# Performance work log

Measured on AMD Instinct MI355X. Metric: run time of the kernel, lower is better.

## Reference

```python
import jax, jax.numpy as jnp
import numpy as np
import math

S, B, D = 2048, 2, 1024
H = 16
DH = D // H
WIN = 256
DIL = 1


def setup_inputs() -> dict:
    key = jax.random.key(0)
    ks = jax.random.split(key, 10)
    std = 1.0 / math.sqrt(D)
    return {
        "x": jax.random.normal(ks[0], (S, B, D), jnp.float32),
        "beta": jax.random.normal(ks[1], (H,), jnp.float32) * 0.02,
        "Wq": jax.random.normal(ks[2], (D, D), jnp.float32) * std,
        "bq": jnp.zeros((D,), jnp.float32),
        "Wk": jax.random.normal(ks[3], (D, D), jnp.float32) * std,
        "bk": jnp.zeros((D,), jnp.float32),
        "Wv": jax.random.normal(ks[4], (D, D), jnp.float32) * std,
        "bv": jnp.zeros((D,), jnp.float32),
        "Wo": jax.random.normal(ks[5], (D, D), jnp.float32) * std,
        "bo": jnp.zeros((D,), jnp.float32),
    }


def _split_heads(t):
    # (S, B, D) -> (B*H, S, DH), matching rearrange 's b (h d) -> (b h) s d'
    return t.reshape(S, B, H, DH).transpose(1, 2, 0, 3).reshape(B * H, S, DH)


def reference(x, beta, Wq, bq, Wk, bk, Wv, bv, Wo, bo):
    q = _split_heads(x @ Wq + bq)
    k = _split_heads(x @ Wk + bk)
    v = _split_heads(x @ Wv + bv)

    # per-head learnable temperature: q / (sqrt(d_head) * exp(beta))
    beta_exp = jnp.tile(jnp.exp(beta), B)  # (B*H,), head index = z % H
    q = q / (jnp.sqrt(jnp.asarray(DH, x.dtype)) * beta_exp)[:, None, None]

    # causal dilated windowed mask
    idx = jnp.arange(S)
    diff = idx[:, None] - idx[None, :]
    allowed = (diff >= 0) & (diff <= DIL * (WIN - 1)) & (diff % DIL == 0)
    mask = jnp.where(allowed, jnp.asarray(0.0, x.dtype), jnp.asarray(-jnp.inf, x.dtype))

    scores = jnp.einsum('zqd,zkd->zqk', q, k) + mask[None]
    # attention sink: extra zero-logit column absorbing probability mass
    scores = jnp.concatenate([scores, jnp.zeros((B * H, S, 1), scores.dtype)], axis=-1)
    attn = jax.nn.softmax(scores, axis=-1)[..., :-1]

    out = jnp.einsum('zqk,zkd->zqd', attn, v)
    # (B*H, S, DH) -> (S, B, D)
    out = out.reshape(B, H, S, DH).transpose(2, 0, 1, 3).reshape(S, B, D)
    return out @ Wo + bo
```

## Files before the change

kernel.cpp:

```cpp
#include <hip/hip_runtime.h>
#include <math.h>

#define S_LEN  2048
#define BATCH  2
#define DM     1024
#define NHEAD  16
#define DHEAD  64
#define WIN    256
#define MROWS  4096

#define KP   72
#define PPAD 68

#define BM 256
#define BN 192
#define BK 64

#define OM 128
#define ON 128

typedef __attribute__((ext_vector_type(8))) short bf16x8;
typedef __attribute__((ext_vector_type(4))) float f32x4;

__device__ __forceinline__ unsigned short f2b(float f) {
    unsigned int u = __float_as_uint(f);
    return (unsigned short)((u + 0x7fffu + ((u >> 16) & 1u)) >> 16);
}
__device__ __forceinline__ void gld16(const void* g, void* l) {
    __builtin_amdgcn_global_load_lds(
        (const __attribute__((address_space(1))) void*)g,
        (__attribute__((address_space(3))) void*)l, 16, 0, 0);
}
__device__ __forceinline__ bf16x8 pack8(float4 a, float4 b) {
    bf16x8 r;
    r[0] = (short)f2b(a.x); r[1] = (short)f2b(a.y);
    r[2] = (short)f2b(a.z); r[3] = (short)f2b(a.w);
    r[4] = (short)f2b(b.x); r[5] = (short)f2b(b.y);
    r[6] = (short)f2b(b.z); r[7] = (short)f2b(b.w);
    return r;
}

__global__ __launch_bounds__(256)
void cvtx(const float* __restrict__ x, unsigned short* __restrict__ xb)
{
    const int i = (blockIdx.x * 256 + threadIdx.x) * 4;
    float4 f = *(const float4*)(x + i);
    ushort4 o; o.x = f2b(f.x); o.y = f2b(f.y); o.z = f2b(f.z); o.w = f2b(f.w);
    *(ushort4*)(xb + i) = o;
}

__global__ __launch_bounds__(256)
void twcvt4(const float* __restrict__ W0, const float* __restrict__ W1,
            const float* __restrict__ W2, const float* __restrict__ W3,
            unsigned short* __restrict__ T0, unsigned short* __restrict__ T1,
            unsigned short* __restrict__ T2, unsigned short* __restrict__ T3)
{
    const int zz = blockIdx.z;
    const float* W = (zz == 0) ? W0 : (zz == 1) ? W1 : (zz == 2) ? W2 : W3;
    unsigned short* WT = (zz == 0) ? T0 : (zz == 1) ? T1 : (zz == 2) ? T2 : T3;

    __shared__ float t32[32][33];
    const int bx = blockIdx.x * 32;
    const int by = blockIdx.y * 32;
    const int c  = threadIdx.x & 31;
    const int r0 = threadIdx.x >> 5;
#pragma unroll
    for (int p = 0; p < 4; ++p)
        t32[r0 + 8 * p][c] = W[(size_t)(by + r0 + 8 * p) * DM + bx + c];
    __syncthreads();
#pragma unroll
    for (int p = 0; p < 4; ++p)
        WT[(size_t)(bx + r0 + 8 * p) * DM + by + c] = f2b(t32[c][r0 + 8 * p]);
}

__global__ __launch_bounds__(512, 2)
void gemm_qkv(const unsigned short* __restrict__ A,
              const unsigned short* __restrict__ BT,
              const float* __restrict__ b0,
              const float* __restrict__ b1,
              const float* __restrict__ b2,
              const float* __restrict__ beta,
              unsigned short* __restrict__ Cb)
{
    __shared__ unsigned short Ab[2][BM * BK];
    __shared__ unsigned short Bb[2][BN * BK];

    const int t   = threadIdx.x;
    const int ln  = t & 63;
    const int wv  = t >> 6;
    const int wr  = wv & 3;
    const int wc  = wv >> 2;
    const int m16 = ln & 15;
    const int g   = ln >> 4;
    const int sw  = m16 & 7;

    const int rowBase = blockIdx.y * BM;
    const int colBase = blockIdx.x * BN;

    const int sr  = t >> 3;
    const int scx = (t & 7) ^ (sr & 7);
    const size_t gOff = (size_t)sr * DM + scx * 8;
    const int    ldOff = t * 8;

    f32x4 acc[4][6];
#pragma unroll
    for (int u = 0; u < 4; ++u)
#pragma unroll
        for (int v = 0; v < 6; ++v)
            acc[u][v] = (f32x4){0.f, 0.f, 0.f, 0.f};

    {
        const unsigned short* a0 = A  + (size_t)rowBase * DM + gOff;
        const unsigned short* bt = BT + (size_t)colBase * DM + gOff;
#pragma unroll
        for (int cb = 0; cb < 3; ++cb)
            gld16(bt + (size_t)cb * 64 * DM, &Bb[0][cb * 4096 + ldOff]);
#pragma unroll
        for (int ca = 0; ca < 4; ++ca)
            gld16(a0 + (size_t)ca * 64 * DM, &Ab[0][ca * 4096 + ldOff]);
        asm volatile("s_waitcnt vmcnt(0)" ::: "memory");
        __builtin_amdgcn_s_barrier();
        __builtin_amdgcn_sched_barrier(0);
    }

    for (int kt = 0; kt < DM / BK; ++kt) {
        const int cur = kt & 1;
        const unsigned short* Ac = Ab[cur];
        const unsigned short* Bc = Bb[cur];
        unsigned short* An = Ab[cur ^ 1];
        unsigned short* Bn = Bb[cur ^ 1];
        const bool hn = (kt < DM / BK - 1);
        const unsigned short* aS = A  + (size_t)rowBase * DM + (kt + 1) * BK + gOff;
        const unsigned short* bS = BT + (size_t)colBase * DM + (kt + 1) * BK + gOff;

        bf16x8 af0[4], bf0[6];
#pragma unroll
        for (int u = 0; u < 4; ++u)
            af0[u] = *(const bf16x8*)&Ac[(wr * 64 + u * 16 + m16) * BK + ((g ^ sw) * 8)];
#pragma unroll
        for (int v = 0; v < 6; ++v)
            bf0[v] = *(const bf16x8*)&Bc[(wc * 96 + v * 16 + m16) * BK + ((g ^ sw) * 8)];

        if (hn) {
            gld16(bS,                    &Bn[ldOff]);
            gld16(bS + (size_t)64 * DM,  &Bn[4096 + ldOff]);
            gld16(bS + (size_t)128 * DM, &Bn[2 * 4096 + ldOff]);
            gld16(aS,                    &An[ldOff]);
            gld16(aS + (size_t)64 * DM,  &An[4096 + ldOff]);
            gld16(aS + (size_t)128 * DM, &An[2 * 4096 + ldOff]);
            gld16(aS + (size_t)192 * DM, &An[3 * 4096 + ldOff]);
        }

        __builtin_amdgcn_s_setprio(1);
#pragma unroll
        for (int u = 0; u < 4; ++u)
#pragma unroll
            for (int v = 0; v < 6; ++v)
                acc[u][v] = __builtin_amdgcn_mfma_f32_16x16x32_bf16(
                    af0[u], bf0[v], acc[u][v], 0, 0, 0);
        __builtin_amdgcn_s_setprio(0);

        bf16x8 af1[4], bf1[6];
#pragma unroll
        for (int u = 0; u < 4; ++u)
            af1[u] = *(const bf16x8*)&Ac[(wr * 64 + u * 16 + m16) * BK + (((4 | g) ^ sw) * 8)];
#pragma unroll
        for (int v = 0; v < 6; ++v)
            bf1[v] = *(const bf16x8*)&Bc[(wc * 96 + v * 16 + m16) * BK + (((4 | g) ^ sw) * 8)];

        __builtin_amdgcn_s_setprio(1);
#pragma unroll
        for (int u = 0; u < 4; ++u)
#pragma unroll
            for (int v = 0; v < 6; ++v)
                acc[u][v] = __builtin_amdgcn_mfma_f32_16x16x32_bf16(
                    af1[u], bf1[v], acc[u][v], 0, 0, 0);
        __builtin_amdgcn_s_setprio(0);

        if (hn)
            asm volatile("s_waitcnt vmcnt(0)" ::: "memory");
        __builtin_amdgcn_s_barrier();
        __builtin_amdgcn_sched_barrier(0);
    }

    const int q4 = g * 4;
#pragma unroll
    for (int v = 0; v < 6; ++v) {
        const int col = colBase + wc * 96 + v * 16 + m16;
        const int sec = col >> 10;
        const int h   = (col >> 6) & (NHEAD - 1);
        const int dh  = col & 63;
        if (sec < 2) {
            const float bi = (sec == 0 ? b0 : b1)[col & (DM - 1)];
            const float sc = (sec == 0) ? 0.125f * __expf(-beta[h]) : 1.0f;
            unsigned short* base = Cb + (size_t)sec * MROWS * DM;
#pragma unroll
            for (int u = 0; u < 4; ++u)
#pragma unroll
                for (int r = 0; r < 4; ++r) {
                    const int row = rowBase + wr * 64 + u * 16 + q4 + r;
                    const int s = row >> 1, bb = row & 1;
                    const int z = bb * NHEAD + h;
                    base[((size_t)z * S_LEN + s) * DHEAD + dh] =
                        f2b((acc[u][v][r] + bi) * sc);
                }
        } else {
            unsigned short* vtb = Cb + (size_t)2 * MROWS * DM;
            const float bi = b2[col & (DM - 1)];
#pragma unroll
            for (int u = 0; u < 4; ++u) {
                const int row0 = rowBase + wr * 64 + u * 16 + q4;
                const int s0   = row0 >> 1;
                ushort2 p0, p1;
                p0.x = f2b(acc[u][v][0] + bi);
                p0.y = f2b(acc[u][v][2] + bi);
                p1.x = f2b(acc[u][v][1] + bi);
                p1.y = f2b(acc[u][v][3] + bi);
                *(ushort2*)(vtb + ((size_t)(h * DHEAD + dh) * S_LEN + s0)) = p0;
                *(ushort2*)(vtb + ((size_t)((NHEAD + h) * DHEAD + dh) * S_LEN + s0)) = p1;
            }
        }
    }
}

__global__ __launch_bounds__(256, 2)
void gemm_out(const unsigned short* __restrict__ A,
              const unsigned short* __restrict__ BT,
              const float* __restrict__ bias,
              float* __restrict__ Cf)
{
    __shared__ unsigned short As[2][OM * BK];
    __shared__ unsigned short Bs[2][ON * BK];

    const int t  = threadIdx.x;
    const int wv = t >> 6, ln = t & 63;
    const int wr = wv >> 1, wc = wv & 1;
    const int m16 = ln & 15, g = ln >> 4;
    const int sw  = m16 & 7;

    const int rowBase = blockIdx.y * OM;
    const int colBase = blockIdx.x * ON;

    const int sr  = t >> 3;
    const int scx = (t & 7) ^ (sr & 7);
    const size_t gOff = (size_t)sr * DM + scx * 8;
    const int    ldOff = t * 8;

    f32x4 acc[4][4];
#pragma unroll
    for (int u = 0; u < 4; ++u)
#pragma unroll
        for (int v = 0; v < 4; ++v)
            acc[u][v] = (f32x4){0.f, 0.f, 0.f, 0.f};

    {
        const unsigned short* a0 = A  + (size_t)rowBase * DM + gOff;
        const unsigned short* bt = BT + (size_t)colBase * DM + gOff;
#pragma unroll
        for (int ca = 0; ca < 2; ++ca)
#pragma unroll
            for (int hf = 0; hf < 2; ++hf)
                gld16(a0 + (size_t)(ca * 64 + hf * 32) * DM,
                      &As[0][ca * 4096 + hf * 2048 + ldOff]);
#pragma unroll
        for (int cb = 0; cb < 2; ++cb)
#pragma unroll
            for (int hf = 0; hf < 2; ++hf)
                gld16(bt + (size_t)(cb * 64 + hf * 32) * DM,
                      &Bs[0][cb * 4096 + hf * 2048 + ldOff]);
        asm volatile("s_waitcnt vmcnt(0)" ::: "memory");
        __builtin_amdgcn_s_barrier();
        __builtin_amdgcn_sched_barrier(0);
    }

    for (int kt = 0; kt < DM / BK; ++kt) {
        const int cur = kt & 1;
        const unsigned short* Ac = As[cur];
        const unsigned short* Bc = Bs[cur];
        unsigned short* An = As[cur ^ 1];
        unsigned short* Bn = Bs[cur ^ 1];
        const bool hn = (kt < DM / BK - 1);
        const unsigned short* aS = A  + (size_t)rowBase * DM + (kt + 1) * BK + gOff;
        const unsigned short* bS = BT + (size_t)colBase * DM + (kt + 1) * BK + gOff;

        bf16x8 af0[4], bf0[4];
#pragma unroll
        for (int u = 0; u < 4; ++u)
            af0[u] = *(const bf16x8*)&Ac[(wr * 64 + u * 16 + m16) * BK + ((g ^ sw) * 8)];
#pragma unroll
        for (int v = 0; v < 4; ++v)
            bf0[v] = *(const bf16x8*)&Bc[(wc * 64 + v * 16 + m16) * BK + ((g ^ sw) * 8)];

        if (hn) {
#pragma unroll
            for (int ca = 0; ca < 2; ++ca)
#pragma unroll
                for (int hf = 0; hf < 2; ++hf)
                    gld16(aS + (size_t)(ca * 64 + hf * 32) * DM,
                          &An[ca * 4096 + hf * 2048 + ldOff]);
#pragma unroll
            for (int cb = 0; cb < 2; ++cb)
#pragma unroll
                for (int hf = 0; hf < 2; ++hf)
                    gld16(bS + (size_t)(cb * 64 + hf * 32) * DM,
                          &Bn[cb * 4096 + hf * 2048 + ldOff]);
        }

        __builtin_amdgcn_s_setprio(1);
#pragma unroll
        for (int u = 0; u < 4; ++u)
#pragma unroll
            for (int v = 0; v < 4; ++v)
                acc[u][v] = __builtin_amdgcn_mfma_f32_16x16x32_bf16(
                    af0[u], bf0[v], acc[u][v], 0, 0, 0);
        __builtin_amdgcn_s_setprio(0);

        bf16x8 af1[4], bf1[4];
#pragma unroll
        for (int u = 0; u < 4; ++u)
            af1[u] = *(const bf16x8*)&Ac[(wr * 64 + u * 16 + m16) * BK + (((4 | g) ^ sw) * 8)];
#pragma unroll
        for (int v = 0; v < 4; ++v)
            bf1[v] = *(const bf16x8*)&Bc[(wc * 64 + v * 16 + m16) * BK + (((4 | g) ^ sw) * 8)];

        __builtin_amdgcn_s_setprio(1);
#pragma unroll
        for (int u = 0; u < 4; ++u)
#pragma unroll
            for (int v = 0; v < 4; ++v)
                acc[u][v] = __builtin_amdgcn_mfma_f32_16x16x32_bf16(
                    af1[u], bf1[v], acc[u][v], 0, 0, 0);
        __builtin_amdgcn_s_setprio(0);

        if (hn)
            asm volatile("s_waitcnt vmcnt(0)" ::: "memory");
        __builtin_amdgcn_s_barrier();
        __builtin_amdgcn_sched_barrier(0);
    }

    const int q4 = g * 4;
#pragma unroll
    for (int v = 0; v < 4; ++v) {
        const int col = colBase + wc * 64 + v * 16 + m16;
        const float bi = bias[col];
#pragma unroll
        for (int u = 0; u < 4; ++u)
#pragma unroll
            for (int r = 0; r < 4; ++r) {
                const int row = rowBase + wr * 64 + u * 16 + q4 + r;
                Cf[(size_t)row * DM + col] = acc[u][v][r] + bi;
            }
    }
}

__global__ __launch_bounds__(256, 4)
void attn_mfma(const unsigned short* __restrict__ q,
               const unsigned short* __restrict__ k,
               const unsigned short* __restrict__ vt,
               unsigned short* __restrict__ ao)
{
    __shared__ unsigned short Ks[64 * KP];
    __shared__ unsigned short Vs[64 * KP];
    __shared__ float Ps[64][PPAD];

    const int t   = threadIdx.x;
    const int wv  = t >> 6, ln = t & 63;
    const int m16 = ln & 15, g = ln >> 4;
    const int z   = blockIdx.y;
    const int q0  = blockIdx.x * 64;
    const size_t zbase = (size_t)z * S_LEN * DHEAD;

    const unsigned short* qrow = q + zbase + (size_t)(q0 + wv * 16 + m16) * DHEAD;
    bf16x8 qf0 = *(const bf16x8*)(qrow + g * 8);
    bf16x8 qf1 = *(const bf16x8*)(qrow + 32 + g * 8);

    f32x4 oacc[4];
#pragma unroll
    for (int v4 = 0; v4 < 4; ++v4) oacc[v4] = (f32x4){0.f, 0.f, 0.f, 0.f};
    float lr[4];
#pragma unroll
    for (int r = 0; r < 4; ++r) lr[r] = 1.f;

    for (int c = 0; c < 5; ++c) {
        const int kb = q0 - 256 + c * 64;
        if (kb < 0) continue;
        __syncthreads();

#pragma unroll
        for (int i = 0; i < 2; ++i) {
            const int id  = t + 256 * i;
            const int row = id >> 3;
            const int co  = (id & 7) * 8;
            *(bf16x8*)&Ks[row * KP + co] =
                *(const bf16x8*)(k + zbase + (size_t)(kb + row) * DHEAD + co);
            *(bf16x8*)&Vs[row * KP + co] =
                *(const bf16x8*)(vt + ((size_t)z * DHEAD + row) * S_LEN + kb + co);
        }
        __syncthreads();

        f32x4 sacc[4];
#pragma unroll
        for (int v4 = 0; v4 < 4; ++v4) {
            sacc[v4] = (f32x4){0.f, 0.f, 0.f, 0.f};
            bf16x8 kf0 = *(const bf16x8*)&Ks[(v4 * 16 + m16) * KP + g * 8];
            sacc[v4] = __builtin_amdgcn_mfma_f32_16x16x32_bf16(qf0, kf0, sacc[v4], 0, 0, 0);
            bf16x8 kf1 = *(const bf16x8*)&Ks[(v4 * 16 + m16) * KP + 32 + g * 8];
            sacc[v4] = __builtin_amdgcn_mfma_f32_16x16x32_bf16(qf1, kf1, sacc[v4], 0, 0, 0);
        }

        const bool mhi = (c == 4), mlo = (c == 0);
#pragma unroll
        for (int r = 0; r < 4; ++r) {
            const int ig = q0 + wv * 16 + g * 4 + r;
            float rsum = 0.f;
#pragma unroll
            for (int v4 = 0; v4 < 4; ++v4) {
                const int jg = kb + v4 * 16 + m16;
                float x = sacc[v4][r];
                const bool valid = (!mhi || jg <= ig) && (!mlo || jg >= ig - (WIN - 1));
                x = valid ? x : -1e30f;
                const float pp = __expf(x);
                Ps[wv * 16 + g * 4 + r][v4 * 16 + m16] = pp;
                rsum += pp;
            }
#pragma unroll
            for (int off = 1; off < 16; off <<= 1)
                rsum += __shfl_xor(rsum, off, 64);
            lr[r] += rsum;
        }
        __syncthreads();

        const float* prow = &Ps[wv * 16 + m16][0];
        bf16x8 pf0 = pack8(*(const float4*)(prow + g * 8),
                           *(const float4*)(prow + g * 8 + 4));
        bf16x8 pf1 = pack8(*(const float4*)(prow + 32 + g * 8),
                           *(const float4*)(prow + 32 + g * 8 + 4));
#pragma unroll
        for (int v4 = 0; v4 < 4; ++v4) {
            bf16x8 vf0 = *(const bf16x8*)&Vs[(v4 * 16 + m16) * KP + g * 8];
            oacc[v4] = __builtin_amdgcn_mfma_f32_16x16x32_bf16(pf0, vf0, oacc[v4], 0, 0, 0);
            bf16x8 vf1 = *(const bf16x8*)&Vs[(v4 * 16 + m16) * KP + 32 + g * 8];
            oacc[v4] = __builtin_amdgcn_mfma_f32_16x16x32_bf16(pf1, vf1, oacc[v4], 0, 0, 0);
        }
    }

    const int bb = z >> 4, h = z & 15;
#pragma unroll
    for (int r = 0; r < 4; ++r) {
        const int ig  = q0 + wv * 16 + g * 4 + r;
        const float inv = 1.f / lr[r];
#pragma unroll
        for (int v4 = 0; v4 < 4; ++v4)
            ao[(size_t)(ig * BATCH + bb) * DM + h * DHEAD + v4 * 16 + m16] =
                f2b(oacc[v4][r] * inv);
    }
}

extern "C" void kernel_launch(void* const* d_in, const int* in_sizes, int n_in,
                              void* d_out, int out_size, void* d_ws, size_t ws_size,
                              hipStream_t stream)
{
    const float* x    = (const float*)d_in[0];
    const float* beta = (const float*)d_in[1];
    const float* Wq   = (const float*)d_in[2];
    const float* bq   = (const float*)d_in[3];
    const float* Wk   = (const float*)d_in[4];
    const float* bk   = (const float*)d_in[5];
    const float* Wv   = (const float*)d_in[6];
    const float* bv   = (const float*)d_in[7];
    const float* Wo   = (const float*)d_in[8];
    const float* bo   = (const float*)d_in[9];
    float* out = (float*)d_out;

    unsigned short* w = (unsigned short*)d_ws;
    const size_t seg = (size_t)MROWS * DM;
    unsigned short* qb  = w;
    unsigned short* kb  = w + seg;
    unsigned short* vtb = w + 2 * seg;
    unsigned short* ab  = w + 3 * seg;
    unsigned short* xb  = w + 4 * seg;
    unsigned short* wtq = w + 5 * seg;
    unsigned short* wtk = wtq + (size_t)DM * DM;
    unsigned short* wtv = wtk + (size_t)DM * DM;
    unsigned short* wto = wtv + (size_t)DM * DM;

    cvtx<<<4096, 256, 0, stream>>>(x, xb);
    twcvt4<<<dim3(32, 32, 4), 256, 0, stream>>>(Wq, Wk, Wv, Wo, wtq, wtk, wtv, wto);

    gemm_qkv<<<dim3(3072 / BN, MROWS / BM), 512, 0, stream>>>(
        xb, wtq, bq, bk, bv, beta, qb);

    attn_mfma<<<dim3(S_LEN / 64, BATCH * NHEAD), 256, 0, stream>>>(qb, kb, vtb, ab);

    gemm_out<<<dim3(DM / ON, MROWS / OM), 256, 0, stream>>>(ab, wto, bo, out);
}
```

Measured before the change: 169.4 us.

## Double-buffer K/V with async LDS loads in attention; halve output GEMM tile width

The attention kernel now stages K and V chunks into double-buffered, XOR-swizzled LDS via direct global-to-LDS loads. The next chunk is prefetched while the current one is computed, and fully masked leading chunks are skipped up front. A block-wide barrier after the probability write is replaced with a wave-local LDS wait, since each wave reads only its own rows. The output projection GEMM tile narrows from 128 to 64 columns to launch more blocks. This trades more LDS per attention block (lower occupancy bound) and less reuse per GEMM block for better overlap and fill.

```diff
diff --git a/kernel.cpp b/kernel.cpp
--- a/kernel.cpp
+++ b/kernel.cpp
@@ -9,7 +9,6 @@
 #define WIN    256
 #define MROWS  4096
 
-#define KP   72
 #define PPAD 68
 
 #define BM 256
@@ -17,7 +16,7 @@
 #define BK 64
 
 #define OM 128
-#define ON 128
+#define ON 64
 
 typedef __attribute__((ext_vector_type(8))) short bf16x8;
 typedef __attribute__((ext_vector_type(4))) float f32x4;
@@ -246,28 +245,22 @@
     const size_t gOff = (size_t)sr * DM + scx * 8;
     const int    ldOff = t * 8;
 
-    f32x4 acc[4][4];
+    f32x4 acc[4][2];
 #pragma unroll
     for (int u = 0; u < 4; ++u)
 #pragma unroll
-        for (int v = 0; v < 4; ++v)
+        for (int v = 0; v < 2; ++v)
             acc[u][v] = (f32x4){0.f, 0.f, 0.f, 0.f};
 
     {
         const unsigned short* a0 = A  + (size_t)rowBase * DM + gOff;
         const unsigned short* bt = BT + (size_t)colBase * DM + gOff;
 #pragma unroll
-        for (int ca = 0; ca < 2; ++ca)
-#pragma unroll
-            for (int hf = 0; hf < 2; ++hf)
-                gld16(a0 + (size_t)(ca * 64 + hf * 32) * DM,
-                      &As[0][ca * 4096 + hf * 2048 + ldOff]);
-#pragma unroll
-        for (int cb = 0; cb < 2; ++cb)
-#pragma unroll
-            for (int hf = 0; hf < 2; ++hf)
-                gld16(bt + (size_t)(cb * 64 + hf * 32) * DM,
-                      &Bs[0][cb * 4096 + hf * 2048 + ldOff]);
+        for (int j = 0; j < 4; ++j)
+            gld16(a0 + (size_t)(j * 32) * DM, &As[0][j * 2048 + ldOff]);
+#pragma unroll
+        for (int j = 0; j < 2; ++j)
+            gld16(bt + (size_t)(j * 32) * DM, &Bs[0][j * 2048 + ldOff]);
         asm volatile("s_waitcnt vmcnt(0)" ::: "memory");
         __builtin_amdgcn_s_barrier();
         __builtin_amdgcn_sched_barrier(0);
@@ -283,51 +276,45 @@
         const unsigned short* aS = A  + (size_t)rowBase * DM + (kt + 1) * BK + gOff;
         const unsigned short* bS = BT + (size_t)colBase * DM + (kt + 1) * BK + gOff;
 
-        bf16x8 af0[4], bf0[4];
+        bf16x8 af0[4], bf0[2];
 #pragma unroll
         for (int u = 0; u < 4; ++u)
             af0[u] = *(const bf16x8*)&Ac[(wr * 64 + u * 16 + m16) * BK + ((g ^ sw) * 8)];
 #pragma unroll
-        for (int v = 0; v < 4; ++v)
-            bf0[v] = *(const bf16x8*)&Bc[(wc * 64 + v * 16 + m16) * BK + ((g ^ sw) * 8)];
+        for (int v = 0; v < 2; ++v)
+            bf0[v] = *(const bf16x8*)&Bc[(wc * 32 + v * 16 + m16) * BK + ((g ^ sw) * 8)];
 
         if (hn) {
 #pragma unroll
-            for (int ca = 0; ca < 2; ++ca)
-#pragma unroll
-                for (int hf = 0; hf < 2; ++hf)
-                    gld16(aS + (size_t)(ca * 64 + hf * 32) * DM,
-                          &An[ca * 4096 + hf * 2048 + ldOff]);
-#pragma unroll
-            for (int cb = 0; cb < 2; ++cb)
-#pragma unroll
-                for (int hf = 0; hf < 2; ++hf)
-                    gld16(bS + (size_t)(cb * 64 + hf * 32) * DM,
-                          &Bn[cb * 4096 + hf * 2048 + ldOff]);
+            for (int j = 0; j < 4; ++j)
+                gld16(aS + (size_t)(j * 32) * DM, &An[j * 2048 + ldOff]);
+#pragma unroll
+            for (int j = 0; j < 2; ++j)
+                gld16(bS + (size_t)(j * 32) * DM, &Bn[j * 2048 + ldOff]);
         }
 
         __builtin_amdgcn_s_setprio(1);
 #pragma unroll
         for (int u = 0; u < 4; ++u)
 #pragma unroll
-            for (int v = 0; v < 4; ++v)
+            for (int v = 0; v < 2; ++v)
                 acc[u][v] = __builtin_amdgcn_mfma_f32_16x16x32_bf16(
                     af0[u], bf0[v], acc[u][v], 0, 0, 0);
         __builtin_amdgcn_s_setprio(0);
 
-        bf16x8 af1[4], bf1[4];
+        bf16x8 af1[4], bf1[2];
 #pragma unroll
         for (int u = 0; u < 4; ++u)
             af1[u] = *(const bf16x8*)&Ac[(wr * 64 + u * 16 + m16) * BK + (((4 | g) ^ sw) * 8)];
 #pragma unroll
-        for (int v = 0; v < 4; ++v)
-            bf1[v] = *(const bf16x8*)&Bc[(wc * 64 + v * 16 + m16) * BK + (((4 | g) ^ sw) * 8)];
+        for (int v = 0; v < 2; ++v)
+            bf1[v] = *(const bf16x8*)&Bc[(wc * 32 + v * 16 + m16) * BK + (((4 | g) ^ sw) * 8)];
 
         __builtin_amdgcn_s_setprio(1);
 #pragma unroll
         for (int u = 0; u < 4; ++u)
 #pragma unroll
-            for (int v = 0; v < 4; ++v)
+            for (int v = 0; v < 2; ++v)
                 acc[u][v] = __builtin_amdgcn_mfma_f32_16x16x32_bf16(
                     af1[u], bf1[v], acc[u][v], 0, 0, 0);
         __builtin_amdgcn_s_setprio(0);
@@ -340,8 +327,8 @@
 
     const int q4 = g * 4;
 #pragma unroll
-    for (int v = 0; v < 4; ++v) {
-        const int col = colBase + wc * 64 + v * 16 + m16;
+    for (int v = 0; v < 2; ++v) {
+        const int col = colBase + wc * 32 + v * 16 + m16;
         const float bi = bias[col];
 #pragma unroll
         for (int u = 0; u < 4; ++u)
@@ -353,23 +340,30 @@
     }
 }
 
-__global__ __launch_bounds__(256, 4)
+__global__ __launch_bounds__(256, 3)
 void attn_mfma(const unsigned short* __restrict__ q,
                const unsigned short* __restrict__ k,
                const unsigned short* __restrict__ vt,
                unsigned short* __restrict__ ao)
 {
-    __shared__ unsigned short Ks[64 * KP];
-    __shared__ unsigned short Vs[64 * KP];
+    __shared__ unsigned short Ks[2][64 * 64];
+    __shared__ unsigned short Vs[2][64 * 64];
     __shared__ float Ps[64][PPAD];
 
     const int t   = threadIdx.x;
     const int wv  = t >> 6, ln = t & 63;
     const int m16 = ln & 15, g = ln >> 4;
+    const int sw  = m16 & 7;
     const int z   = blockIdx.y;
     const int q0  = blockIdx.x * 64;
     const size_t zbase = (size_t)z * S_LEN * DHEAD;
 
+    const int sr  = t >> 3;
+    const int scx = (t & 7) ^ (sr & 7);
+    const unsigned short* kS = k  + zbase + (size_t)sr * DHEAD + scx * 8;
+    const unsigned short* vS = vt + ((size_t)z * DHEAD + sr) * S_LEN + scx * 8;
+    const int ldOff = t * 8;
+
     const unsigned short* qrow = q + zbase + (size_t)(q0 + wv * 16 + m16) * DHEAD;
     bf16x8 qf0 = *(const bf16x8*)(qrow + g * 8);
     bf16x8 qf1 = *(const bf16x8*)(qrow + 32 + g * 8);
@@ -381,30 +375,39 @@
 #pragma unroll
     for (int r = 0; r < 4; ++r) lr[r] = 1.f;
 
-    for (int c = 0; c < 5; ++c) {
-        const int kb = q0 - 256 + c * 64;
-        if (kb < 0) continue;
-        __syncthreads();
-
-#pragma unroll
-        for (int i = 0; i < 2; ++i) {
-            const int id  = t + 256 * i;
-            const int row = id >> 3;
-            const int co  = (id & 7) * 8;
-            *(bf16x8*)&Ks[row * KP + co] =
-                *(const bf16x8*)(k + zbase + (size_t)(kb + row) * DHEAD + co);
-            *(bf16x8*)&Vs[row * KP + co] =
-                *(const bf16x8*)(vt + ((size_t)z * DHEAD + row) * S_LEN + kb + co);
-        }
-        __syncthreads();
+    const int c0 = (blockIdx.x < 4) ? (4 - (int)blockIdx.x) : 0;
+
+    {
+        const int kb = q0 - 256 + c0 * 64;
+        gld16(kS + (size_t)kb * DHEAD,        &Ks[0][ldOff]);
+        gld16(kS + (size_t)(kb + 32) * DHEAD, &Ks[0][2048 + ldOff]);
+        gld16(vS + kb,                        &Vs[0][ldOff]);
+        gld16(vS + (size_t)32 * S_LEN + kb,   &Vs[0][2048 + ldOff]);
+        asm volatile("s_waitcnt vmcnt(0)" ::: "memory");
+        __builtin_amdgcn_s_barrier();
+        __builtin_amdgcn_sched_barrier(0);
+    }
+
+    for (int c = c0; c < 5; ++c) {
+        const int cur = (c - c0) & 1;
+        const int kb  = q0 - 256 + c * 64;
+        const bool hn = (c < 4);
+
+        if (hn) {
+            const int kn = kb + 64;
+            gld16(kS + (size_t)kn * DHEAD,        &Ks[cur ^ 1][ldOff]);
+            gld16(kS + (size_t)(kn + 32) * DHEAD, &Ks[cur ^ 1][2048 + ldOff]);
+            gld16(vS + kn,                        &Vs[cur ^ 1][ldOff]);
+            gld16(vS + (size_t)32 * S_LEN + kn,   &Vs[cur ^ 1][2048 + ldOff]);
+        }
 
         f32x4 sacc[4];
 #pragma unroll
         for (int v4 = 0; v4 < 4; ++v4) {
             sacc[v4] = (f32x4){0.f, 0.f, 0.f, 0.f};
-            bf16x8 kf0 = *(const bf16x8*)&Ks[(v4 * 16 + m16) * KP + g * 8];
+            bf16x8 kf0 = *(const bf16x8*)&Ks[cur][(v4 * 16 + m16) * 64 + ((g ^ sw) * 8)];
             sacc[v4] = __builtin_amdgcn_mfma_f32_16x16x32_bf16(qf0, kf0, sacc[v4], 0, 0, 0);
-            bf16x8 kf1 = *(const bf16x8*)&Ks[(v4 * 16 + m16) * KP + 32 + g * 8];
+            bf16x8 kf1 = *(const bf16x8*)&Ks[cur][(v4 * 16 + m16) * 64 + (((4 | g) ^ sw) * 8)];
             sacc[v4] = __builtin_amdgcn_mfma_f32_16x16x32_bf16(qf1, kf1, sacc[v4], 0, 0, 0);
         }
 
@@ -428,7 +431,9 @@
                 rsum += __shfl_xor(rsum, off, 64);
             lr[r] += rsum;
         }
-        __syncthreads();
+
+        asm volatile("s_waitcnt lgkmcnt(0)" ::: "memory");
+        __builtin_amdgcn_sched_barrier(0);
 
         const float* prow = &Ps[wv * 16 + m16][0];
         bf16x8 pf0 = pack8(*(const float4*)(prow + g * 8),
@@ -437,10 +442,16 @@
                            *(const float4*)(prow + 32 + g * 8 + 4));
 #pragma unroll
         for (int v4 = 0; v4 < 4; ++v4) {
-            bf16x8 vf0 = *(const bf16x8*)&Vs[(v4 * 16 + m16) * KP + g * 8];
+            bf16x8 vf0 = *(const bf16x8*)&Vs[cur][(v4 * 16 + m16) * 64 + ((g ^ sw) * 8)];
             oacc[v4] = __builtin_amdgcn_mfma_f32_16x16x32_bf16(pf0, vf0, oacc[v4], 0, 0, 0);
-            bf16x8 vf1 = *(const bf16x8*)&Vs[(v4 * 16 + m16) * KP + 32 + g * 8];
+            bf16x8 vf1 = *(const bf16x8*)&Vs[cur][(v4 * 16 + m16) * 64 + (((4 | g) ^ sw) * 8)];
             oacc[v4] = __builtin_amdgcn_mfma_f32_16x16x32_bf16(pf1, vf1, oacc[v4], 0, 0, 0);
+        }
+
+        if (hn) {
+            asm volatile("s_waitcnt vmcnt(0)" ::: "memory");
+            __builtin_amdgcn_s_barrier();
+            __builtin_amdgcn_sched_barrier(0);
         }
     }
 
```

Result: no change. 170.5 us (+0.6%).
